# Kernel tuning notes

Hardware: AMD Instinct MI355X
Metric: run time of the kernel (lower is better)

Reference implementation:

```python
import jax, jax.numpy as jnp
import numpy as np

D = 1024
H = 16
DH = D // H
L = 128  # max_pos_len
B = 4
T = 1024
SCALE = float(np.sqrt(D / H))


def setup_inputs() -> dict:
    key = jax.random.key(0)
    ks = jax.random.split(key, 9)
    x_q = jax.random.normal(ks[0], (B, T, D), dtype=jnp.float32)
    x_k = jax.random.normal(ks[1], (B, T, D), dtype=jnp.float32)
    x_v = jax.random.normal(ks[2], (B, T, D), dtype=jnp.float32)
    mask = jax.random.randint(ks[3], (B, 1, 1, T), 0, 2) == 1  # bool, True = masked
    Wq = jax.random.normal(ks[4], (D, D), dtype=jnp.float32) * 0.02
    Wk = jax.random.normal(ks[5], (D, D), dtype=jnp.float32) * 0.02
    Wv = jax.random.normal(ks[6], (D, D), dtype=jnp.float32) * 0.02
    Wo = jax.random.normal(ks[7], (D, D), dtype=jnp.float32) * 0.02
    pos_emb = jax.random.normal(ks[8], (2 * L + 1, DH), dtype=jnp.float32)
    return {"x_q": x_q, "x_k": x_k, "x_v": x_v, "mask": mask,
            "Wq": Wq, "Wk": Wk, "Wv": Wv, "Wo": Wo, "pos_emb": pos_emb}


def reference(x_q, x_k, x_v, mask, Wq, Wk, Wv, Wo, pos_emb):
    # nn.Linear(bias=False): y = x @ W.T
    def split_heads(x):  # (B,T,D) -> (B,H,T,DH)
        return x.reshape(B, -1, H, DH).transpose(0, 2, 1, 3)

    Q = split_heads(x_q @ Wq.T)
    K = split_heads(x_k @ Wk.T)
    V = split_heads(x_v @ Wv.T)

    logits = jnp.einsum('bhqd,bhkd->bhqk', Q, K)

    # arrange_char_pos_embedding: indices[q,k] = clamp(k-q, -L, L) + L
    rel = jnp.clip(jnp.arange(T)[None, :] - jnp.arange(T)[:, None], -L, L) + L
    arranged_pos = pos_emb[rel]  # (T_Q, T_K, DH)
    pos_logits = jnp.einsum('bhqd,qkd->bhqk', Q, arranged_pos)

    logits = (logits + pos_logits) / SCALE
    logits = jnp.where(mask, -jnp.inf, logits)  # mask broadcasts (B,1,1,T)
    attn = jax.nn.softmax(logits, axis=-1)  # dropout p=0.0 -> identity

    combined = jnp.einsum('bhqk,bhkd->bhqd', attn, V)
    heads_concat = combined.transpose(0, 2, 1, 3).reshape(B, -1, D)
    return heads_concat @ Wo.T
```

## Files before the change

kernel.cpp:

```cpp
#include <hip/hip_runtime.h>
#include <hip/hip_bf16.h>
#include <stdint.h>

typedef __attribute__((ext_vector_type(8))) short short8;
typedef __attribute__((ext_vector_type(4))) float f32x4;

__device__ __forceinline__ uint16_t f2bf(float f) {
    union { float f; uint32_t u; } v; v.f = f;
    uint32_t r = v.u + 0x7FFF + ((v.u >> 16) & 1);
    return (uint16_t)(r >> 16);
}
__device__ __forceinline__ float bf2f(uint16_t u) {
    union { uint32_t u; float f; } v; v.u = ((uint32_t)u) << 16;
    return v.f;
}

template<int F32>
__device__ __forceinline__ uint4 load8(const void* p, size_t off) {
    if (F32) {
        const float* f = (const float*)p + off;
        float4 f0 = *(const float4*)f;
        float4 f1 = *(const float4*)(f + 4);
        uint4 r;
        r.x = (uint32_t)f2bf(f0.x) | ((uint32_t)f2bf(f0.y) << 16);
        r.y = (uint32_t)f2bf(f0.z) | ((uint32_t)f2bf(f0.w) << 16);
        r.z = (uint32_t)f2bf(f1.x) | ((uint32_t)f2bf(f1.y) << 16);
        r.w = (uint32_t)f2bf(f1.z) | ((uint32_t)f2bf(f1.w) << 16);
        return r;
    } else {
        return *(const uint4*)((const uint16_t*)p + off);
    }
}

#define GLDS(gp, lp) __builtin_amdgcn_global_load_lds( \
    (const __attribute__((address_space(1))) void*)(gp), \
    (__attribute__((address_space(3))) void*)(lp), 16, 0, 0)

__global__ __launch_bounds__(256) void mask_canon(
    const void* __restrict__ raw, int* __restrict__ canon)
{
    __shared__ int flags[3];
    const uint32_t* w = (const uint32_t*)raw;
    const uint8_t* b8 = (const uint8_t*)raw;
    const int t = threadIdx.x;
    if (t < 3) flags[t] = 0;
    __syncthreads();
    int fbyte = 0, ff32 = 0, fodd = 0;
    for (int i = t; i < 1024; i += 256) {
        uint32_t v = w[i];
        if (v != 0u && v != 1u && v != 0x3F800000u) fbyte = 1;
        if (v == 0x3F800000u) ff32 = 1;
        if ((i & 1) && v != 0u) fodd = 1;
    }
    if (fbyte) atomicOr(&flags[0], 1);
    if (ff32)  atomicOr(&flags[1], 1);
    if (fodd)  atomicOr(&flags[2], 1);
    __syncthreads();
    int mode;
    if (flags[0]) mode = 1;
    else if (flags[1]) mode = 0;
    else if (!flags[2]) mode = 2;
    else mode = 0;
    for (int k = t; k < 4096; k += 256) {
        int val;
        if (mode == 1)      val = (b8[k] != 0);
        else if (mode == 2) val = (w[2 * k] != 0u);
        else                val = (w[k] != 0u);
        canon[k] = val;
    }
}

struct CvtSeg { const float* s; uint16_t* d; int n8; };
struct CvtArgs { CvtSeg seg[9]; int nseg; };

__global__ __launch_bounds__(256) void cvt_bf16(CvtArgs a)
{
    const int tid = blockIdx.x * 256 + threadIdx.x;
    const int stride = gridDim.x * 256;
    for (int s = 0; s < a.nseg; ++s) {
        const float* src = a.seg[s].s;
        uint16_t* dst = a.seg[s].d;
        const int n8 = a.seg[s].n8;
        if (src) {
            for (int i = tid; i < n8; i += stride)
                *(uint4*)(dst + (size_t)i * 8) = load8<1>(src, (size_t)i * 8);
        } else {
            const uint4 z = {0u, 0u, 0u, 0u};
            for (int i = tid; i < n8; i += stride)
                *(uint4*)(dst + (size_t)i * 8) = z;
        }
    }
}

template<int AF32>
__device__ __forceinline__ void gemm128_body(
    const void* __restrict__ A, const uint16_t* __restrict__ B,
    void* __restrict__ C, int M, int N, int K, int cm, int bm, int bn,
    uint16_t* As, uint16_t* Bs)
{
    const int t = threadIdx.x;
    const int lane = t & 63, wave = t >> 6;
    const int lrow = lane & 15, quad = lane >> 4;
    const int wr = (wave >> 1) * 64, wc = (wave & 1) * 64;

    const int g_row = wave * 16 + (lane >> 2);
    const int g_col = (lane & 3) * 8;
    const int s_row = t >> 1, s_col = (t & 1) * 16;

    const uint16_t* Ab = (const uint16_t*)A;
    const float*    Af = (const float*)A;

    const f32x4 fz = {0.f, 0.f, 0.f, 0.f};
    f32x4 acc[4][4];
#pragma unroll
    for (int i = 0; i < 4; ++i)
#pragma unroll
        for (int j = 0; j < 4; ++j) acc[i][j] = fz;

    for (int k0 = 0; k0 < K; k0 += 32) {
        uint4 lo, hi;
        if (AF32) {
            size_t off = (size_t)(bm * 128 + s_row) * K + k0 + s_col;
            lo = load8<1>(Af, off);
            hi = load8<1>(Af, off + 8);
        }
        __syncthreads();
        if (AF32) {
            *(uint4*)(As + s_row * 32 + s_col)     = lo;
            *(uint4*)(As + s_row * 32 + s_col + 8) = hi;
        } else {
            GLDS(Ab + (size_t)(bm * 128 + g_row) * K + k0 + g_col,      As + wave * 512);
            GLDS(Ab + (size_t)(bm * 128 + g_row + 64) * K + k0 + g_col, As + wave * 512 + 2048);
        }
        GLDS(B + (size_t)(bn * 128 + g_row) * K + k0 + g_col,      Bs + wave * 512);
        GLDS(B + (size_t)(bn * 128 + g_row + 64) * K + k0 + g_col, Bs + wave * 512 + 2048);
        __syncthreads();

        short8 a[4], b[4];
#pragma unroll
        for (int i = 0; i < 4; ++i)
            a[i] = *(const short8*)(As + (wr + i * 16 + lrow) * 32 + quad * 8);
#pragma unroll
        for (int j = 0; j < 4; ++j)
            b[j] = *(const short8*)(Bs + (wc + j * 16 + lrow) * 32 + quad * 8);
#pragma unroll
        for (int i = 0; i < 4; ++i)
#pragma unroll
            for (int j = 0; j < 4; ++j)
                acc[i][j] = __builtin_amdgcn_mfma_f32_16x16x32_bf16(a[i], b[j], acc[i][j], 0, 0, 0);
    }

    if (cm == 2) {
        __syncthreads();
        uint16_t* scr = As + wave * 1024;
#pragma unroll
        for (int i = 0; i < 4; ++i)
#pragma unroll
            for (int j = 0; j < 4; ++j) {
                uint2 pk;
                pk.x = (uint32_t)f2bf(acc[i][j][0]) | ((uint32_t)f2bf(acc[i][j][1]) << 16);
                pk.y = (uint32_t)f2bf(acc[i][j][2]) | ((uint32_t)f2bf(acc[i][j][3]) << 16);
                *(uint2*)(scr + lrow * 16 + quad * 4) = pk;
                if (lane < 32) {
                    int n = lane >> 1, m8 = (lane & 1) * 8;
                    short8 vv = *(const short8*)(scr + n * 16 + m8);
                    int ng = bn * 128 + wc + j * 16 + n;
                    int hh = ng >> 6, d = ng & 63;
                    int mg = bm * 128 + wr + i * 16;
                    int bb = mg >> 10, tl = (mg & 1023) + m8;
                    *(short8*)((uint16_t*)C +
                        ((((size_t)bb * 16 + hh) * 64 + d) * 1024 + tl)) = vv;
                }
            }
        return;
    }

#pragma unroll
    for (int i = 0; i < 4; ++i)
#pragma unroll
        for (int j = 0; j < 4; ++j)
#pragma unroll
            for (int r = 0; r < 4; ++r) {
                int m = bm * 128 + wr + i * 16 + quad * 4 + r;
                int n = bn * 128 + wc + j * 16 + lrow;
                float val = acc[i][j][r];
                if (cm == 0) {
                    ((float*)C)[(size_t)m * N + n] = val;
                } else {
                    int bb = m >> 10, tt = m & 1023, hh = n >> 6, d = n & 63;
                    ((uint16_t*)C)[(((size_t)bb * 16 + hh) * 1024 + tt) * 64 + d] = f2bf(val);
                }
            }
}

template<int AF32>
__global__ __launch_bounds__(256) void gemm128_qkv(
    const void* __restrict__ xq, const void* __restrict__ xk, const void* __restrict__ xv,
    const uint16_t* __restrict__ Wq, const uint16_t* __restrict__ Wk, const uint16_t* __restrict__ Wv,
    uint16_t* __restrict__ Qh, uint16_t* __restrict__ Khd, uint16_t* __restrict__ Vt)
{
    __shared__ alignas(16) uint16_t As[128 * 32];
    __shared__ alignas(16) uint16_t Bs[128 * 32];
    const int z = blockIdx.z;
    const void* A = (z == 0) ? xq : (z == 1) ? xk : xv;
    const uint16_t* B = (z == 0) ? Wq : (z == 1) ? Wk : Wv;
    void* C = (z == 0) ? (void*)Qh : (z == 1) ? (void*)Khd : (void*)Vt;
    const int cm = (z == 2) ? 2 : 1;
    gemm128_body<AF32>(A, B, C, 4096, 1024, 1024, cm, blockIdx.x, blockIdx.y, As, Bs);
}

__global__ __launch_bounds__(256) void gemm128_single(
    const void* __restrict__ A, const uint16_t* __restrict__ B, void* __restrict__ C,
    int M, int N, int K, int cm)
{
    __shared__ alignas(16) uint16_t As[128 * 32];
    __shared__ alignas(16) uint16_t Bs[128 * 32];
    gemm128_body<0>(A, B, C, M, N, K, cm, blockIdx.x, blockIdx.y, As, Bs);
}

__global__ __launch_bounds__(256) void flash_attn(
    const uint16_t* __restrict__ Qh, const uint16_t* __restrict__ Kh,
    const uint16_t* __restrict__ Vt, const uint16_t* __restrict__ pos,
    const int* __restrict__ mask, uint16_t* __restrict__ comb)
{
    const int blk = blockIdx.x;
    const int bh = blk >> 4;
    const int qt = blk & 15;
    const int b = bh >> 4;
    const int h = bh & 15;
    const int t = threadIdx.x;
    const int lane = t & 63;
    const int wave = t >> 6;
    const int lrow = lane & 15;
    const int quad = lane >> 4;
    const int qb = qt * 64 + wave * 16;

    __shared__ alignas(16) uint16_t Ks[2 * 64 * 32];
    __shared__ alignas(16) uint16_t Vs[2 * 64 * 32];
    __shared__ alignas(16) uint16_t Qpos_l[64][276];
    __shared__ alignas(16) uint16_t Pl[4][16][80];

    const uint16_t* Qp = Qh + ((size_t)bh * 1024 + qb) * 64;
    short8 aq0 = *(const short8*)(Qp + (size_t)lrow * 64 + quad * 8);
    short8 aq1 = *(const short8*)(Qp + (size_t)lrow * 64 + 32 + quad * 8);

    const f32x4 fz = {0.f, 0.f, 0.f, 0.f};

#pragma unroll 4
    for (int nt = 0; nt < 17; ++nt) {
        short8 pb0 = *(const short8*)(pos + (size_t)(nt * 16 + lrow) * 64 + quad * 8);
        short8 pb1 = *(const short8*)(pos + (size_t)(nt * 16 + lrow) * 64 + 32 + quad * 8);
        f32x4 c = __builtin_amdgcn_mfma_f32_16x16x32_bf16(aq0, pb0, fz, 0, 0, 0);
        c = __builtin_amdgcn_mfma_f32_16x16x32_bf16(aq1, pb1, c, 0, 0, 0);
#pragma unroll
        for (int r = 0; r < 4; ++r)
            Qpos_l[wave * 16 + quad * 4 + r][nt * 16 + lrow] = f2bf(c[r]);
    }

    float pcl[4], pch[4];
#pragma unroll
    for (int r = 0; r < 4; ++r) {
        int ql = wave * 16 + quad * 4 + r;
        pcl[r] = bf2f(Qpos_l[ql][0])   * 0.125f;
        pch[r] = bf2f(Qpos_l[ql][256]) * 0.125f;
    }

    const uint16_t* Kp = Kh + (size_t)bh * 65536;
    const uint16_t* Vp = Vt + (size_t)bh * 65536;
    const int* mk = mask + b * 1024;

    const int sg_r = lane >> 2;
    const int sg_c = (lane & 3) * 8;
    const int hw = wave >> 1;
    const int gw = (wave & 1) * 2;

    f32x4 o[4] = {fz, fz, fz, fz};
    float lsum[4] = {0.f, 0.f, 0.f, 0.f};

    for (int kb = 0; kb < 1024; kb += 64) {
        __syncthreads();
#pragma unroll
        for (int gg = 0; gg < 2; ++gg) {
            int g = gw + gg;
            GLDS(Kp + (size_t)(kb + g * 16 + sg_r) * 64 + hw * 32 + sg_c,
                 Ks + hw * 2048 + g * 512);
            GLDS(Vp + (size_t)(g * 16 + sg_r) * 1024 + kb + hw * 32 + sg_c,
                 Vs + hw * 2048 + g * 512);
        }
        __syncthreads();

        f32x4 s[4];
#pragma unroll
        for (int j = 0; j < 4; ++j) {
            short8 k0 = *(const short8*)(Ks + (j * 16 + lrow) * 32 + quad * 8);
            short8 k1 = *(const short8*)(Ks + 2048 + (j * 16 + lrow) * 32 + quad * 8);
            s[j] = __builtin_amdgcn_mfma_f32_16x16x32_bf16(aq0, k0, fz, 0, 0, 0);
            s[j] = __builtin_amdgcn_mfma_f32_16x16x32_bf16(aq1, k1, s[j], 0, 0, 0);
        }

        const int diff = kb - qb;
        if (diff <= -192 || diff >= 144) {
            const bool low = (diff <= -192);
#pragma unroll
            for (int j = 0; j < 4; ++j) {
                const int key = kb + j * 16 + lrow;
                const bool m = (mk[key] != 0);
#pragma unroll
                for (int r = 0; r < 4; ++r) {
                    float pc = low ? pcl[r] : pch[r];
                    float e = m ? 0.f : __expf(__builtin_fmaf(s[j][r], 0.125f, pc));
                    lsum[r] += e;
                    Pl[wave][quad * 4 + r][j * 16 + lrow] = f2bf(e);
                }
            }
        } else {
#pragma unroll
            for (int j = 0; j < 4; ++j) {
                const int key = kb + j * 16 + lrow;
                const bool m = (mk[key] != 0);
#pragma unroll
                for (int r = 0; r < 4; ++r) {
                    int q = qb + quad * 4 + r;
                    int ql = q & 63;
                    int rel = min(max(key - q, -128), 128) + 128;
                    float p = bf2f(Qpos_l[ql][rel]);
                    float e = m ? 0.f : __expf((s[j][r] + p) * 0.125f);
                    lsum[r] += e;
                    Pl[wave][quad * 4 + r][j * 16 + lrow] = f2bf(e);
                }
            }
        }
        short8 ap0 = *(const short8*)(&Pl[wave][lrow][quad * 8]);
        short8 ap1 = *(const short8*)(&Pl[wave][lrow][32 + quad * 8]);

#pragma unroll
        for (int dt = 0; dt < 4; ++dt) {
            short8 v0 = *(const short8*)(Vs + (dt * 16 + lrow) * 32 + quad * 8);
            short8 v1 = *(const short8*)(Vs + 2048 + (dt * 16 + lrow) * 32 + quad * 8);
            o[dt] = __builtin_amdgcn_mfma_f32_16x16x32_bf16(ap0, v0, o[dt], 0, 0, 0);
            o[dt] = __builtin_amdgcn_mfma_f32_16x16x32_bf16(ap1, v1, o[dt], 0, 0, 0);
        }
    }

#pragma unroll
    for (int off = 1; off < 16; off <<= 1)
#pragma unroll
        for (int r = 0; r < 4; ++r)
            lsum[r] += __shfl_xor(lsum[r], off);

    float inv[4];
#pragma unroll
    for (int r = 0; r < 4; ++r) inv[r] = 1.0f / lsum[r];

#pragma unroll
    for (int dt = 0; dt < 4; ++dt)
#pragma unroll
        for (int r = 0; r < 4; ++r) {
            size_t row = (size_t)b * 1024 + qb + quad * 4 + r;
            size_t col = (size_t)h * 64 + dt * 16 + lrow;
            comb[row * 1024 + col] = f2bf(o[dt][r] * inv[r]);
        }
}

extern "C" void kernel_launch(void* const* d_in, const int* in_sizes, int n_in,
                              void* d_out, int out_size, void* d_ws, size_t ws_size,
                              hipStream_t stream)
{
    const float* x_q = (const float*)d_in[0];
    const float* x_k = (const float*)d_in[1];
    const float* x_v = (const float*)d_in[2];
    const void*  msk = d_in[3];
    const float* Wq  = (const float*)d_in[4];
    const float* Wk  = (const float*)d_in[5];
    const float* Wv  = (const float*)d_in[6];
    const float* Wo  = (const float*)d_in[7];
    const float* pos = (const float*)d_in[8];

    char* ws = (char*)d_ws;
    const size_t MB = 1u << 20;
    uint16_t* Qh  = (uint16_t*)(ws);
    uint16_t* Khd = (uint16_t*)(ws + 8 * MB);
    uint16_t* Vt  = (uint16_t*)(ws + 16 * MB);

    const bool big = ws_size >= 60 * MB;
    uint16_t *comb, *Wqb, *Wkb, *Wvb, *Wob, *posb;
    uint16_t *xqb = nullptr, *xkb = nullptr, *xvb = nullptr;
    int* canon;
    if (big) {
        xqb  = (uint16_t*)(ws + 24 * MB);
        xkb  = (uint16_t*)(ws + 32 * MB);
        xvb  = (uint16_t*)(ws + 40 * MB);
        Wqb  = (uint16_t*)(ws + 48 * MB);
        Wkb  = (uint16_t*)(ws + 50 * MB);
        Wvb  = (uint16_t*)(ws + 52 * MB);
        Wob  = (uint16_t*)(ws + 54 * MB);
        posb = (uint16_t*)(ws + 56 * MB);
        canon = (int*)(ws + 56 * MB + 65536);
        comb = xqb;
    } else {
        comb = (uint16_t*)(ws + 24 * MB);
        Wqb  = (uint16_t*)(ws + 32 * MB);
        Wkb  = (uint16_t*)(ws + 34 * MB);
        Wvb  = (uint16_t*)(ws + 36 * MB);
        Wob  = (uint16_t*)(ws + 38 * MB);
        posb = (uint16_t*)(ws + 40 * MB);
        canon = (int*)(ws + 40 * MB + 65536);
    }

    mask_canon<<<dim3(1), dim3(256), 0, stream>>>(msk, canon);

    CvtArgs ca{};
    int ns = 0;
    if (big) {
        ca.seg[ns++] = {x_q, xqb, 524288};
        ca.seg[ns++] = {x_k, xkb, 524288};
        ca.seg[ns++] = {x_v, xvb, 524288};
    }
    ca.seg[ns++] = {Wq, Wqb, 131072};
    ca.seg[ns++] = {Wk, Wkb, 131072};
    ca.seg[ns++] = {Wv, Wvb, 131072};
    ca.seg[ns++] = {Wo, Wob, 131072};
    ca.seg[ns++] = {pos, posb, 2056};
    ca.seg[ns++] = {nullptr, posb + 16448, 120};
    ca.nseg = ns;
    cvt_bf16<<<dim3(512), dim3(256), 0, stream>>>(ca);

    if (big)
        gemm128_qkv<0><<<dim3(32, 8, 3), dim3(256), 0, stream>>>(
            xqb, xkb, xvb, Wqb, Wkb, Wvb, Qh, Khd, Vt);
    else
        gemm128_qkv<1><<<dim3(32, 8, 3), dim3(256), 0, stream>>>(
            x_q, x_k, x_v, Wqb, Wkb, Wvb, Qh, Khd, Vt);

    flash_attn<<<dim3(1024), dim3(256), 0, stream>>>(Qh, Khd, Vt, posb, canon, comb);

    gemm128_single<<<dim3(32, 8), dim3(256), 0, stream>>>(
        comb, Wob, d_out, 4096, 1024, 1024, 0);
}
```

Measured before the change: 258.9 us.

## Halve flash-attention key tile to 32 and fold mask canonicalization into convert kernel

The flash attention loop now processes 32 keys per iteration instead of 64, with smaller K/V shared buffers and one MFMA per output tile for PV. The constant-position-bias thresholds are adjusted to the new tile size. Shared memory shrinks, which may allow more blocks per CU, but it doubles the loop iterations and barriers. The mask canonicalization kernel is merged into block 0 of the bf16 conversion kernel to save a launch.

```diff
diff --git a/kernel.cpp b/kernel.cpp
--- a/kernel.cpp
+++ b/kernel.cpp
@@ -36,45 +36,42 @@
     (const __attribute__((address_space(1))) void*)(gp), \
     (__attribute__((address_space(3))) void*)(lp), 16, 0, 0)
 
-__global__ __launch_bounds__(256) void mask_canon(
-    const void* __restrict__ raw, int* __restrict__ canon)
-{
-    __shared__ int flags[3];
-    const uint32_t* w = (const uint32_t*)raw;
-    const uint8_t* b8 = (const uint8_t*)raw;
-    const int t = threadIdx.x;
-    if (t < 3) flags[t] = 0;
-    __syncthreads();
-    int fbyte = 0, ff32 = 0, fodd = 0;
-    for (int i = t; i < 1024; i += 256) {
-        uint32_t v = w[i];
-        if (v != 0u && v != 1u && v != 0x3F800000u) fbyte = 1;
-        if (v == 0x3F800000u) ff32 = 1;
-        if ((i & 1) && v != 0u) fodd = 1;
-    }
-    if (fbyte) atomicOr(&flags[0], 1);
-    if (ff32)  atomicOr(&flags[1], 1);
-    if (fodd)  atomicOr(&flags[2], 1);
-    __syncthreads();
-    int mode;
-    if (flags[0]) mode = 1;
-    else if (flags[1]) mode = 0;
-    else if (!flags[2]) mode = 2;
-    else mode = 0;
-    for (int k = t; k < 4096; k += 256) {
-        int val;
-        if (mode == 1)      val = (b8[k] != 0);
-        else if (mode == 2) val = (w[2 * k] != 0u);
-        else                val = (w[k] != 0u);
-        canon[k] = val;
-    }
-}
-
 struct CvtSeg { const float* s; uint16_t* d; int n8; };
-struct CvtArgs { CvtSeg seg[9]; int nseg; };
+struct CvtArgs { CvtSeg seg[9]; int nseg; const void* mraw; int* mcanon; };
 
 __global__ __launch_bounds__(256) void cvt_bf16(CvtArgs a)
 {
+    if (blockIdx.x == 0) {
+        __shared__ int flags[3];
+        const uint32_t* w = (const uint32_t*)a.mraw;
+        const uint8_t* b8 = (const uint8_t*)a.mraw;
+        const int t = threadIdx.x;
+        if (t < 3) flags[t] = 0;
+        __syncthreads();
+        int fbyte = 0, ff32 = 0, fodd = 0;
+        for (int i = t; i < 1024; i += 256) {
+            uint32_t v = w[i];
+            if (v != 0u && v != 1u && v != 0x3F800000u) fbyte = 1;
+            if (v == 0x3F800000u) ff32 = 1;
+            if ((i & 1) && v != 0u) fodd = 1;
+        }
+        if (fbyte) atomicOr(&flags[0], 1);
+        if (ff32)  atomicOr(&flags[1], 1);
+        if (fodd)  atomicOr(&flags[2], 1);
+        __syncthreads();
+        int mode;
+        if (flags[0]) mode = 1;
+        else if (flags[1]) mode = 0;
+        else if (!flags[2]) mode = 2;
+        else mode = 0;
+        for (int k = t; k < 4096; k += 256) {
+            int val;
+            if (mode == 1)      val = (b8[k] != 0);
+            else if (mode == 2) val = (w[2 * k] != 0u);
+            else                val = (w[k] != 0u);
+            a.mcanon[k] = val;
+        }
+    }
     const int tid = blockIdx.x * 256 + threadIdx.x;
     const int stride = gridDim.x * 256;
     for (int s = 0; s < a.nseg; ++s) {
@@ -235,10 +232,10 @@
     const int quad = lane >> 4;
     const int qb = qt * 64 + wave * 16;
 
-    __shared__ alignas(16) uint16_t Ks[2 * 64 * 32];
-    __shared__ alignas(16) uint16_t Vs[2 * 64 * 32];
-    __shared__ alignas(16) uint16_t Qpos_l[64][276];
-    __shared__ alignas(16) uint16_t Pl[4][16][80];
+    __shared__ alignas(16) uint16_t Ks[2048];
+    __shared__ alignas(16) uint16_t Vs[2048];
+    __shared__ alignas(16) uint16_t Qpos_l[64][274];
+    __shared__ alignas(16) uint16_t Pl[4][16][72];
 
     const uint16_t* Qp = Qh + ((size_t)bh * 1024 + qb) * 64;
     short8 aq0 = *(const short8*)(Qp + (size_t)lrow * 64 + quad * 8);
@@ -269,40 +266,35 @@
     const uint16_t* Vp = Vt + (size_t)bh * 65536;
     const int* mk = mask + b * 1024;
 
-    const int sg_r = lane >> 2;
-    const int sg_c = (lane & 3) * 8;
-    const int hw = wave >> 1;
-    const int gw = (wave & 1) * 2;
+    const int sr = lane >> 2;
+    const int sc = (lane & 3) * 8;
+    const int khalf = wave >> 1, ksub = wave & 1;
 
     f32x4 o[4] = {fz, fz, fz, fz};
     float lsum[4] = {0.f, 0.f, 0.f, 0.f};
 
-    for (int kb = 0; kb < 1024; kb += 64) {
-        __syncthreads();
-#pragma unroll
-        for (int gg = 0; gg < 2; ++gg) {
-            int g = gw + gg;
-            GLDS(Kp + (size_t)(kb + g * 16 + sg_r) * 64 + hw * 32 + sg_c,
-                 Ks + hw * 2048 + g * 512);
-            GLDS(Vp + (size_t)(g * 16 + sg_r) * 1024 + kb + hw * 32 + sg_c,
-                 Vs + hw * 2048 + g * 512);
-        }
-        __syncthreads();
-
-        f32x4 s[4];
-#pragma unroll
-        for (int j = 0; j < 4; ++j) {
+    for (int kb = 0; kb < 1024; kb += 32) {
+        __syncthreads();
+        GLDS(Kp + (size_t)(kb + ksub * 16 + sr) * 64 + khalf * 32 + sc,
+             Ks + (khalf * 2 + ksub) * 512);
+        GLDS(Vp + (size_t)(wave * 16 + sr) * 1024 + kb + sc,
+             Vs + wave * 512);
+        __syncthreads();
+
+        f32x4 s[2];
+#pragma unroll
+        for (int j = 0; j < 2; ++j) {
             short8 k0 = *(const short8*)(Ks + (j * 16 + lrow) * 32 + quad * 8);
-            short8 k1 = *(const short8*)(Ks + 2048 + (j * 16 + lrow) * 32 + quad * 8);
+            short8 k1 = *(const short8*)(Ks + 1024 + (j * 16 + lrow) * 32 + quad * 8);
             s[j] = __builtin_amdgcn_mfma_f32_16x16x32_bf16(aq0, k0, fz, 0, 0, 0);
             s[j] = __builtin_amdgcn_mfma_f32_16x16x32_bf16(aq1, k1, s[j], 0, 0, 0);
         }
 
         const int diff = kb - qb;
-        if (diff <= -192 || diff >= 144) {
-            const bool low = (diff <= -192);
-#pragma unroll
-            for (int j = 0; j < 4; ++j) {
+        if (diff <= -159 || diff >= 143) {
+            const bool low = (diff <= -159);
+#pragma unroll
+            for (int j = 0; j < 2; ++j) {
                 const int key = kb + j * 16 + lrow;
                 const bool m = (mk[key] != 0);
 #pragma unroll
@@ -315,7 +307,7 @@
             }
         } else {
 #pragma unroll
-            for (int j = 0; j < 4; ++j) {
+            for (int j = 0; j < 2; ++j) {
                 const int key = kb + j * 16 + lrow;
                 const bool m = (mk[key] != 0);
 #pragma unroll
@@ -330,15 +322,12 @@
                 }
             }
         }
-        short8 ap0 = *(const short8*)(&Pl[wave][lrow][quad * 8]);
-        short8 ap1 = *(const short8*)(&Pl[wave][lrow][32 + quad * 8]);
+        short8 ap = *(const short8*)(&Pl[wave][lrow][quad * 8]);
 
 #pragma unroll
         for (int dt = 0; dt < 4; ++dt) {
-            short8 v0 = *(const short8*)(Vs + (dt * 16 + lrow) * 32 + quad * 8);
-            short8 v1 = *(const short8*)(Vs + 2048 + (dt * 16 + lrow) * 32 + quad * 8);
-            o[dt] = __builtin_amdgcn_mfma_f32_16x16x32_bf16(ap0, v0, o[dt], 0, 0, 0);
-            o[dt] = __builtin_amdgcn_mfma_f32_16x16x32_bf16(ap1, v1, o[dt], 0, 0, 0);
+            short8 v = *(const short8*)(Vs + (dt * 16 + lrow) * 32 + quad * 8);
+            o[dt] = __builtin_amdgcn_mfma_f32_16x16x32_bf16(ap, v, o[dt], 0, 0, 0);
         }
     }
 
@@ -407,8 +396,6 @@
         canon = (int*)(ws + 40 * MB + 65536);
     }
 
-    mask_canon<<<dim3(1), dim3(256), 0, stream>>>(msk, canon);
-
     CvtArgs ca{};
     int ns = 0;
     if (big) {
@@ -423,6 +410,8 @@
     ca.seg[ns++] = {pos, posb, 2056};
     ca.seg[ns++] = {nullptr, posb + 16448, 120};
     ca.nseg = ns;
+    ca.mraw = msk;
+    ca.mcanon = canon;
     cvt_bf16<<<dim3(512), dim3(256), 0, stream>>>(ca);
 
     if (big)
```

Result: slower. 269.8 us (+4.2%).

## Load fp32 activations directly into LDS in QKV GEMM, fold mask into convert kernel

Applied to the files above, without the earlier changes.

The QKV projection GEMM now pulls fp32 activation tiles straight into shared memory with async global-to-LDS loads and converts them to bf16 when reading fragments. This removes the separate pre-conversion pass over the inputs and its extra global round trip. The mask canonicalisation kernel is merged into block 0 of the weight-convert kernel to save a launch, and the convert grid shrinks. Attention LDS padding is also adjusted. In exchange, fp32 tiles double the LDS footprint and bandwidth per tile, and the fragment reads now redo the conversion inside the hot loop.

```diff
diff --git a/kernel.cpp b/kernel.cpp
--- a/kernel.cpp
+++ b/kernel.cpp
@@ -36,45 +36,42 @@
     (const __attribute__((address_space(1))) void*)(gp), \
     (__attribute__((address_space(3))) void*)(lp), 16, 0, 0)
 
-__global__ __launch_bounds__(256) void mask_canon(
-    const void* __restrict__ raw, int* __restrict__ canon)
-{
-    __shared__ int flags[3];
-    const uint32_t* w = (const uint32_t*)raw;
-    const uint8_t* b8 = (const uint8_t*)raw;
-    const int t = threadIdx.x;
-    if (t < 3) flags[t] = 0;
-    __syncthreads();
-    int fbyte = 0, ff32 = 0, fodd = 0;
-    for (int i = t; i < 1024; i += 256) {
-        uint32_t v = w[i];
-        if (v != 0u && v != 1u && v != 0x3F800000u) fbyte = 1;
-        if (v == 0x3F800000u) ff32 = 1;
-        if ((i & 1) && v != 0u) fodd = 1;
-    }
-    if (fbyte) atomicOr(&flags[0], 1);
-    if (ff32)  atomicOr(&flags[1], 1);
-    if (fodd)  atomicOr(&flags[2], 1);
-    __syncthreads();
-    int mode;
-    if (flags[0]) mode = 1;
-    else if (flags[1]) mode = 0;
-    else if (!flags[2]) mode = 2;
-    else mode = 0;
-    for (int k = t; k < 4096; k += 256) {
-        int val;
-        if (mode == 1)      val = (b8[k] != 0);
-        else if (mode == 2) val = (w[2 * k] != 0u);
-        else                val = (w[k] != 0u);
-        canon[k] = val;
-    }
-}
-
 struct CvtSeg { const float* s; uint16_t* d; int n8; };
-struct CvtArgs { CvtSeg seg[9]; int nseg; };
+struct CvtArgs { CvtSeg seg[6]; int nseg; const void* mraw; int* mcanon; };
 
 __global__ __launch_bounds__(256) void cvt_bf16(CvtArgs a)
 {
+    if (blockIdx.x == 0) {
+        __shared__ int flags[3];
+        const uint32_t* w = (const uint32_t*)a.mraw;
+        const uint8_t* b8 = (const uint8_t*)a.mraw;
+        const int t = threadIdx.x;
+        if (t < 3) flags[t] = 0;
+        __syncthreads();
+        int fbyte = 0, ff32 = 0, fodd = 0;
+        for (int i = t; i < 1024; i += 256) {
+            uint32_t v = w[i];
+            if (v != 0u && v != 1u && v != 0x3F800000u) fbyte = 1;
+            if (v == 0x3F800000u) ff32 = 1;
+            if ((i & 1) && v != 0u) fodd = 1;
+        }
+        if (fbyte) atomicOr(&flags[0], 1);
+        if (ff32)  atomicOr(&flags[1], 1);
+        if (fodd)  atomicOr(&flags[2], 1);
+        __syncthreads();
+        int mode;
+        if (flags[0]) mode = 1;
+        else if (flags[1]) mode = 0;
+        else if (!flags[2]) mode = 2;
+        else mode = 0;
+        for (int k = t; k < 4096; k += 256) {
+            int val;
+            if (mode == 1)      val = (b8[k] != 0);
+            else if (mode == 2) val = (w[2 * k] != 0u);
+            else                val = (w[k] != 0u);
+            a.mcanon[k] = val;
+        }
+    }
     const int tid = blockIdx.x * 256 + threadIdx.x;
     const int stride = gridDim.x * 256;
     for (int s = 0; s < a.nseg; ++s) {
@@ -92,12 +89,22 @@
     }
 }
 
-template<int AF32>
-__device__ __forceinline__ void gemm128_body(
-    const void* __restrict__ A, const uint16_t* __restrict__ B,
-    void* __restrict__ C, int M, int N, int K, int cm, int bm, int bn,
-    uint16_t* As, uint16_t* Bs)
+__global__ __launch_bounds__(256) void gemm128_qkv(
+    const float* __restrict__ xq, const float* __restrict__ xk, const float* __restrict__ xv,
+    const uint16_t* __restrict__ Wq, const uint16_t* __restrict__ Wk, const uint16_t* __restrict__ Wv,
+    uint16_t* __restrict__ Qh, uint16_t* __restrict__ Khd, uint16_t* __restrict__ Vt)
 {
+    __shared__ alignas(16) float    AsF[128 * 32];
+    __shared__ alignas(16) uint16_t Bs[128 * 32];
+
+    const int z = blockIdx.z;
+    const float* A = (z == 0) ? xq : (z == 1) ? xk : xv;
+    const uint16_t* B = (z == 0) ? Wq : (z == 1) ? Wk : Wv;
+    uint16_t* C = (z == 0) ? Qh : (z == 1) ? Khd : Vt;
+    const int cm = (z == 2) ? 2 : 1;
+    const int bm = blockIdx.x, bn = blockIdx.y;
+    const int K = 1024;
+
     const int t = threadIdx.x;
     const int lane = t & 63, wave = t >> 6;
     const int lrow = lane & 15, quad = lane >> 4;
@@ -105,10 +112,8 @@
 
     const int g_row = wave * 16 + (lane >> 2);
     const int g_col = (lane & 3) * 8;
-    const int s_row = t >> 1, s_col = (t & 1) * 16;
-
-    const uint16_t* Ab = (const uint16_t*)A;
-    const float*    Af = (const float*)A;
+    const int a_r = lane >> 3;
+    const int a_c = (lane & 7) * 4;
 
     const f32x4 fz = {0.f, 0.f, 0.f, 0.f};
     f32x4 acc[4][4];
@@ -118,19 +123,12 @@
         for (int j = 0; j < 4; ++j) acc[i][j] = fz;
 
     for (int k0 = 0; k0 < K; k0 += 32) {
-        uint4 lo, hi;
-        if (AF32) {
-            size_t off = (size_t)(bm * 128 + s_row) * K + k0 + s_col;
-            lo = load8<1>(Af, off);
-            hi = load8<1>(Af, off + 8);
-        }
-        __syncthreads();
-        if (AF32) {
-            *(uint4*)(As + s_row * 32 + s_col)     = lo;
-            *(uint4*)(As + s_row * 32 + s_col + 8) = hi;
-        } else {
-            GLDS(Ab + (size_t)(bm * 128 + g_row) * K + k0 + g_col,      As + wave * 512);
-            GLDS(Ab + (size_t)(bm * 128 + g_row + 64) * K + k0 + g_col, As + wave * 512 + 2048);
+        __syncthreads();
+#pragma unroll
+        for (int g = 0; g < 4; ++g) {
+            int rbase = (wave * 4 + g) * 8;
+            GLDS(A + (size_t)(bm * 128 + rbase + a_r) * K + k0 + a_c,
+                 AsF + (size_t)(wave * 4 + g) * 256);
         }
         GLDS(B + (size_t)(bn * 128 + g_row) * K + k0 + g_col,      Bs + wave * 512);
         GLDS(B + (size_t)(bn * 128 + g_row + 64) * K + k0 + g_col, Bs + wave * 512 + 2048);
@@ -138,8 +136,17 @@
 
         short8 a[4], b[4];
 #pragma unroll
-        for (int i = 0; i < 4; ++i)
-            a[i] = *(const short8*)(As + (wr + i * 16 + lrow) * 32 + quad * 8);
+        for (int i = 0; i < 4; ++i) {
+            const float* rp = AsF + (wr + i * 16 + lrow) * 32 + quad * 8;
+            float4 f0 = *(const float4*)rp;
+            float4 f1 = *(const float4*)(rp + 4);
+            uint4 pk;
+            pk.x = (uint32_t)f2bf(f0.x) | ((uint32_t)f2bf(f0.y) << 16);
+            pk.y = (uint32_t)f2bf(f0.z) | ((uint32_t)f2bf(f0.w) << 16);
+            pk.z = (uint32_t)f2bf(f1.x) | ((uint32_t)f2bf(f1.y) << 16);
+            pk.w = (uint32_t)f2bf(f1.z) | ((uint32_t)f2bf(f1.w) << 16);
+            a[i] = *(short8*)&pk;
+        }
 #pragma unroll
         for (int j = 0; j < 4; ++j)
             b[j] = *(const short8*)(Bs + (wc + j * 16 + lrow) * 32 + quad * 8);
@@ -152,7 +159,7 @@
 
     if (cm == 2) {
         __syncthreads();
-        uint16_t* scr = As + wave * 1024;
+        uint16_t* scr = (uint16_t*)AsF + wave * 1024;
 #pragma unroll
         for (int i = 0; i < 4; ++i)
 #pragma unroll
@@ -168,8 +175,7 @@
                     int hh = ng >> 6, d = ng & 63;
                     int mg = bm * 128 + wr + i * 16;
                     int bb = mg >> 10, tl = (mg & 1023) + m8;
-                    *(short8*)((uint16_t*)C +
-                        ((((size_t)bb * 16 + hh) * 64 + d) * 1024 + tl)) = vv;
+                    *(short8*)(C + ((((size_t)bb * 16 + hh) * 64 + d) * 1024 + tl)) = vv;
                 }
             }
         return;
@@ -183,39 +189,65 @@
             for (int r = 0; r < 4; ++r) {
                 int m = bm * 128 + wr + i * 16 + quad * 4 + r;
                 int n = bn * 128 + wc + j * 16 + lrow;
-                float val = acc[i][j][r];
-                if (cm == 0) {
-                    ((float*)C)[(size_t)m * N + n] = val;
-                } else {
-                    int bb = m >> 10, tt = m & 1023, hh = n >> 6, d = n & 63;
-                    ((uint16_t*)C)[(((size_t)bb * 16 + hh) * 1024 + tt) * 64 + d] = f2bf(val);
-                }
+                int bb = m >> 10, tt = m & 1023, hh = n >> 6, d = n & 63;
+                C[(((size_t)bb * 16 + hh) * 1024 + tt) * 64 + d] = f2bf(acc[i][j][r]);
             }
 }
 
-template<int AF32>
-__global__ __launch_bounds__(256) void gemm128_qkv(
-    const void* __restrict__ xq, const void* __restrict__ xk, const void* __restrict__ xv,
-    const uint16_t* __restrict__ Wq, const uint16_t* __restrict__ Wk, const uint16_t* __restrict__ Wv,
-    uint16_t* __restrict__ Qh, uint16_t* __restrict__ Khd, uint16_t* __restrict__ Vt)
+__global__ __launch_bounds__(256) void gemm128_single(
+    const uint16_t* __restrict__ A, const uint16_t* __restrict__ B,
+    float* __restrict__ C, int M, int N, int K)
 {
     __shared__ alignas(16) uint16_t As[128 * 32];
     __shared__ alignas(16) uint16_t Bs[128 * 32];
-    const int z = blockIdx.z;
-    const void* A = (z == 0) ? xq : (z == 1) ? xk : xv;
-    const uint16_t* B = (z == 0) ? Wq : (z == 1) ? Wk : Wv;
-    void* C = (z == 0) ? (void*)Qh : (z == 1) ? (void*)Khd : (void*)Vt;
-    const int cm = (z == 2) ? 2 : 1;
-    gemm128_body<AF32>(A, B, C, 4096, 1024, 1024, cm, blockIdx.x, blockIdx.y, As, Bs);
-}
-
-__global__ __launch_bounds__(256) void gemm128_single(
-    const void* __restrict__ A, const uint16_t* __restrict__ B, void* __restrict__ C,
-    int M, int N, int K, int cm)
-{
-    __shared__ alignas(16) uint16_t As[128 * 32];
-    __shared__ alignas(16) uint16_t Bs[128 * 32];
-    gemm128_body<0>(A, B, C, M, N, K, cm, blockIdx.x, blockIdx.y, As, Bs);
+
+    const int t = threadIdx.x;
+    const int lane = t & 63, wave = t >> 6;
+    const int lrow = lane & 15, quad = lane >> 4;
+    const int wr = (wave >> 1) * 64, wc = (wave & 1) * 64;
+    const int g_row = wave * 16 + (lane >> 2);
+    const int g_col = (lane & 3) * 8;
+    const int bm = blockIdx.x, bn = blockIdx.y;
+
+    const f32x4 fz = {0.f, 0.f, 0.f, 0.f};
+    f32x4 acc[4][4];
+#pragma unroll
+    for (int i = 0; i < 4; ++i)
+#pragma unroll
+        for (int j = 0; j < 4; ++j) acc[i][j] = fz;
+
+    for (int k0 = 0; k0 < K; k0 += 32) {
+        __syncthreads();
+        GLDS(A + (size_t)(bm * 128 + g_row) * K + k0 + g_col,      As + wave * 512);
+        GLDS(A + (size_t)(bm * 128 + g_row + 64) * K + k0 + g_col, As + wave * 512 + 2048);
+        GLDS(B + (size_t)(bn * 128 + g_row) * K + k0 + g_col,      Bs + wave * 512);
+        GLDS(B + (size_t)(bn * 128 + g_row + 64) * K + k0 + g_col, Bs + wave * 512 + 2048);
+        __syncthreads();
+
+        short8 a[4], b[4];
+#pragma unroll
+        for (int i = 0; i < 4; ++i)
+            a[i] = *(const short8*)(As + (wr + i * 16 + lrow) * 32 + quad * 8);
+#pragma unroll
+        for (int j = 0; j < 4; ++j)
+            b[j] = *(const short8*)(Bs + (wc + j * 16 + lrow) * 32 + quad * 8);
+#pragma unroll
+        for (int i = 0; i < 4; ++i)
+#pragma unroll
+            for (int j = 0; j < 4; ++j)
+                acc[i][j] = __builtin_amdgcn_mfma_f32_16x16x32_bf16(a[i], b[j], acc[i][j], 0, 0, 0);
+    }
+
+#pragma unroll
+    for (int i = 0; i < 4; ++i)
+#pragma unroll
+        for (int j = 0; j < 4; ++j)
+#pragma unroll
+            for (int r = 0; r < 4; ++r) {
+                int m = bm * 128 + wr + i * 16 + quad * 4 + r;
+                int n = bn * 128 + wc + j * 16 + lrow;
+                C[(size_t)m * N + n] = acc[i][j][r];
+            }
 }
 
 __global__ __launch_bounds__(256) void flash_attn(
@@ -237,8 +269,8 @@
 
     __shared__ alignas(16) uint16_t Ks[2 * 64 * 32];
     __shared__ alignas(16) uint16_t Vs[2 * 64 * 32];
-    __shared__ alignas(16) uint16_t Qpos_l[64][276];
-    __shared__ alignas(16) uint16_t Pl[4][16][80];
+    __shared__ alignas(16) uint16_t Qpos_l[64][274];
+    __shared__ alignas(16) uint16_t Pl[4][16][72];
 
     const uint16_t* Qp = Qh + ((size_t)bh * 1024 + qb) * 64;
     short8 aq0 = *(const short8*)(Qp + (size_t)lrow * 64 + quad * 8);
@@ -378,44 +410,19 @@
 
     char* ws = (char*)d_ws;
     const size_t MB = 1u << 20;
-    uint16_t* Qh  = (uint16_t*)(ws);
-    uint16_t* Khd = (uint16_t*)(ws + 8 * MB);
-    uint16_t* Vt  = (uint16_t*)(ws + 16 * MB);
-
-    const bool big = ws_size >= 60 * MB;
-    uint16_t *comb, *Wqb, *Wkb, *Wvb, *Wob, *posb;
-    uint16_t *xqb = nullptr, *xkb = nullptr, *xvb = nullptr;
-    int* canon;
-    if (big) {
-        xqb  = (uint16_t*)(ws + 24 * MB);
-        xkb  = (uint16_t*)(ws + 32 * MB);
-        xvb  = (uint16_t*)(ws + 40 * MB);
-        Wqb  = (uint16_t*)(ws + 48 * MB);
-        Wkb  = (uint16_t*)(ws + 50 * MB);
-        Wvb  = (uint16_t*)(ws + 52 * MB);
-        Wob  = (uint16_t*)(ws + 54 * MB);
-        posb = (uint16_t*)(ws + 56 * MB);
-        canon = (int*)(ws + 56 * MB + 65536);
-        comb = xqb;
-    } else {
-        comb = (uint16_t*)(ws + 24 * MB);
-        Wqb  = (uint16_t*)(ws + 32 * MB);
-        Wkb  = (uint16_t*)(ws + 34 * MB);
-        Wvb  = (uint16_t*)(ws + 36 * MB);
-        Wob  = (uint16_t*)(ws + 38 * MB);
-        posb = (uint16_t*)(ws + 40 * MB);
-        canon = (int*)(ws + 40 * MB + 65536);
-    }
-
-    mask_canon<<<dim3(1), dim3(256), 0, stream>>>(msk, canon);
+    uint16_t* Qh   = (uint16_t*)(ws);
+    uint16_t* Khd  = (uint16_t*)(ws + 8 * MB);
+    uint16_t* Vt   = (uint16_t*)(ws + 16 * MB);
+    uint16_t* comb = (uint16_t*)(ws + 24 * MB);
+    uint16_t* Wqb  = (uint16_t*)(ws + 32 * MB);
+    uint16_t* Wkb  = (uint16_t*)(ws + 34 * MB);
+    uint16_t* Wvb  = (uint16_t*)(ws + 36 * MB);
+    uint16_t* Wob  = (uint16_t*)(ws + 38 * MB);
+    uint16_t* posb = (uint16_t*)(ws + 40 * MB);
+    int*      canon = (int*)(ws + 40 * MB + 65536);
 
     CvtArgs ca{};
     int ns = 0;
-    if (big) {
-        ca.seg[ns++] = {x_q, xqb, 524288};
-        ca.seg[ns++] = {x_k, xkb, 524288};
-        ca.seg[ns++] = {x_v, xvb, 524288};
-    }
     ca.seg[ns++] = {Wq, Wqb, 131072};
     ca.seg[ns++] = {Wk, Wkb, 131072};
     ca.seg[ns++] = {Wv, Wvb, 131072};
@@ -423,17 +430,15 @@
     ca.seg[ns++] = {pos, posb, 2056};
     ca.seg[ns++] = {nullptr, posb + 16448, 120};
     ca.nseg = ns;
-    cvt_bf16<<<dim3(512), dim3(256), 0, stream>>>(ca);
-
-    if (big)
-        gemm128_qkv<0><<<dim3(32, 8, 3), dim3(256), 0, stream>>>(
-            xqb, xkb, xvb, Wqb, Wkb, Wvb, Qh, Khd, Vt);
-    else
-        gemm128_qkv<1><<<dim3(32, 8, 3), dim3(256), 0, stream>>>(
-            x_q, x_k, x_v, Wqb, Wkb, Wvb, Qh, Khd, Vt);
+    ca.mraw = msk;
+    ca.mcanon = canon;
+    cvt_bf16<<<dim3(128), dim3(256), 0, stream>>>(ca);
+
+    gemm128_qkv<<<dim3(32, 8, 3), dim3(256), 0, stream>>>(
+        x_q, x_k, x_v, Wqb, Wkb, Wvb, Qh, Khd, Vt);
 
     flash_attn<<<dim3(1024), dim3(256), 0, stream>>>(Qh, Khd, Vt, posb, canon, comb);
 
     gemm128_single<<<dim3(32, 8), dim3(256), 0, stream>>>(
-        comb, Wob, d_out, 4096, 1024, 1024, 0);
-}
+        comb, Wob, (float*)d_out, 4096, 1024, 1024);
+}
```

Result: slower. 305.4 us (+18.0%).
